# Performance work log

Measured on AMD Instinct MI355X. Metric: run time of the kernel, lower is better.

The kernel has to match this reference:

```python
import jax, jax.numpy as jnp
import numpy as np

NUM_GRAPHS = 512  # number of segments (graphs) in the batch
N_NODES = 200000
HIDDEN = 256


def setup_inputs() -> dict:
    key = jax.random.key(0)
    ks = jax.random.split(key, 8)
    x = jax.random.normal(ks[0], (N_NODES, HIDDEN), dtype=jnp.float32)
    batch = jnp.sort(jax.random.randint(ks[1], (N_NODES,), 0, NUM_GRAPHS, dtype=jnp.int32))
    h4 = HIDDEN // 4
    w1 = jax.random.normal(ks[2], (HIDDEN, h4), dtype=jnp.float32) * (1.0 / np.sqrt(HIDDEN))
    b1 = jnp.zeros((h4,), dtype=jnp.float32)
    w2 = jax.random.normal(ks[3], (h4, 1), dtype=jnp.float32) * (1.0 / np.sqrt(h4))
    b2 = jnp.zeros((1,), dtype=jnp.float32)
    wp = jax.random.normal(ks[4], (3 * HIDDEN, HIDDEN), dtype=jnp.float32) * (1.0 / np.sqrt(3 * HIDDEN))
    bp = jnp.zeros((HIDDEN,), dtype=jnp.float32)
    gamma = jnp.ones((HIDDEN,), dtype=jnp.float32)
    beta = jnp.zeros((HIDDEN,), dtype=jnp.float32)
    return {"x": x, "batch": batch, "w1": w1, "b1": b1, "w2": w2, "b2": b2,
            "wp": wp, "bp": bp, "gamma": gamma, "beta": beta}


def reference(x, batch, w1, b1, w2, b2, wp, bp, gamma, beta):
    G = NUM_GRAPHS
    # --- global mean pool ---
    seg_sum = jax.ops.segment_sum(x, batch, num_segments=G)  # [G, H]
    counts = jax.ops.segment_sum(jnp.ones((x.shape[0],), x.dtype), batch, num_segments=G)
    z_mean = seg_sum / jnp.maximum(counts, 1.0)[:, None]
    # --- global max pool ---
    z_max = jax.ops.segment_max(x, batch, num_segments=G)
    z_max = jnp.where(jnp.isfinite(z_max), z_max, 0.0)  # guard empty segments
    # --- global attention pool (PyG GlobalAttention) ---
    gate = jnp.maximum(x @ w1 + b1, 0.0) @ w2 + b2  # [N, 1]
    g = gate[:, 0]
    g_max = jax.ops.segment_max(g, batch, num_segments=G)
    g_max = jnp.where(jnp.isfinite(g_max), g_max, 0.0)
    e = jnp.exp(g - g_max[batch])
    denom = jax.ops.segment_sum(e, batch, num_segments=G)
    w = e / jnp.maximum(denom, 1e-16)[batch]  # scatter-softmax weights [N]
    z_attn = jax.ops.segment_sum(w[:, None] * x, batch, num_segments=G)
    # --- concat + proj + layernorm ---
    z = jnp.concatenate([z_mean, z_max, z_attn], axis=-1)  # [G, 3H]
    y = z @ wp + bp  # [G, H]
    mu = jnp.mean(y, axis=-1, keepdims=True)
    var = jnp.mean(jnp.square(y - mu), axis=-1, keepdims=True)
    yhat = (y - mu) * jax.lax.rsqrt(var + 1e-5)
    return yhat * gamma + beta
```

## Files before the change

### kernel.cpp

```cpp
#include <hip/hip_runtime.h>
#include <math.h>

#define N_NODES 200000
#define NGRAPH  512
#define HID     256

typedef __attribute__((ext_vector_type(8))) short s16x8;
typedef __attribute__((ext_vector_type(4))) float f32x4;

__device__ __forceinline__ unsigned short f2bf_rne(float f) {
  unsigned int u = __float_as_uint(f);
  return (unsigned short)((u + 0x7fffu + ((u >> 16) & 1u)) >> 16);
}

__global__ __launch_bounds__(256, 2) void fused_gate_pool(
    const float* __restrict__ x,
    const int* __restrict__ batch,
    const float* __restrict__ w1,
    const float* __restrict__ b1,
    const float* __restrict__ w2,
    const float* __restrict__ b2,
    float* __restrict__ zbuf)
{
  __shared__ __align__(16) float chunk_f[64 * 256];
  __shared__ int sbounds[2];
  __shared__ float sm[4], sd[4];

  const int tid = threadIdx.x;
  const int w = tid >> 6;
  const int lane = tid & 63;
  const int q = lane >> 4;
  const int c = lane & 15;

  if (tid < 2) {
    int target = blockIdx.x + tid;
    int lo = 0, hi = N_NODES;
    while (lo < hi) { int mid = (lo + hi) >> 1; if (batch[mid] < target) lo = mid + 1; else hi = mid; }
    sbounds[tid] = lo;
  }

  {
    const float4* src = (const float4*)w1;
    float4* dst = (float4*)chunk_f;
    for (int i = tid; i < 4096; i += 256) dst[i] = src[i];
  }
  __syncthreads();
  s16x8 bh[8][4];
#pragma unroll
  for (int kt = 0; kt < 8; ++kt)
#pragma unroll
    for (int nt = 0; nt < 4; ++nt) {
      s16x8 v;
#pragma unroll
      for (int j = 0; j < 8; ++j)
        v[j] = (short)f2bf_rne(chunk_f[(kt * 32 + q * 8 + j) * 64 + nt * 16 + c]);
      bh[kt][nt] = v;
    }
  float b1v[4], w2v[4];
#pragma unroll
  for (int nt = 0; nt < 4; ++nt) { b1v[nt] = b1[nt * 16 + c]; w2v[nt] = w2[nt * 16 + c]; }
  const float b2v = b2[0];
  const int s = sbounds[0], e = sbounds[1];
  const int cnt = e - s;
  __syncthreads();

  f32x4 sum = (f32x4){0.f, 0.f, 0.f, 0.f};
  f32x4 mx  = (f32x4){-INFINITY, -INFINITY, -INFINITY, -INFINITY};
  f32x4 at  = (f32x4){0.f, 0.f, 0.f, 0.f};
  float den = 0.f, m = -INFINITY;

  const int nchunks = (cnt + 63) >> 6;
  for (int ch = 0; ch < nchunks; ++ch) {
    const int base = s + (ch << 6);
    const int nvalid = min(64, e - base);

#pragma unroll
    for (int it = 0; it < 16; ++it) {
      int row = it * 4 + w;
      if (row < nvalid) {
        const float* gsrc = x + (size_t)(base + row) * HID + lane * 4;
        float* ldst = &chunk_f[row * 256 + lane * 4];
        __builtin_amdgcn_global_load_lds(
            (const __attribute__((address_space(1))) unsigned int*)gsrc,
            (__attribute__((address_space(3))) unsigned int*)ldst, 16, 0, 0);
      }
    }
    __syncthreads();

    const int lim = min(16, nvalid - w * 16);
    if (lim > 0) {
      f32x4 acc[4];
#pragma unroll
      for (int nt = 0; nt < 4; ++nt) acc[nt] = (f32x4){0.f, 0.f, 0.f, 0.f};
#pragma unroll
      for (int kt = 0; kt < 8; ++kt) {
        const float* ar = &chunk_f[(w * 16 + c) * 256 + kt * 32 + q * 8];
        float4 f0 = *(const float4*)ar;
        float4 f1 = *(const float4*)(ar + 4);
        s16x8 ah;
        ah[0] = (short)f2bf_rne(f0.x); ah[1] = (short)f2bf_rne(f0.y);
        ah[2] = (short)f2bf_rne(f0.z); ah[3] = (short)f2bf_rne(f0.w);
        ah[4] = (short)f2bf_rne(f1.x); ah[5] = (short)f2bf_rne(f1.y);
        ah[6] = (short)f2bf_rne(f1.z); ah[7] = (short)f2bf_rne(f1.w);
#pragma unroll
        for (int nt = 0; nt < 4; ++nt)
          acc[nt] = __builtin_amdgcn_mfma_f32_16x16x32_bf16(ah, bh[kt][nt], acc[nt], 0, 0, 0);
      }

      float gr[4];
#pragma unroll
      for (int r = 0; r < 4; ++r) {
        float sv = 0.f;
#pragma unroll
        for (int nt = 0; nt < 4; ++nt) {
          float h = acc[nt][r] + b1v[nt];
          h = h > 0.f ? h : 0.f;
          sv += h * w2v[nt];
        }
        sv += __shfl_xor(sv, 1, 64);
        sv += __shfl_xor(sv, 2, 64);
        sv += __shfl_xor(sv, 4, 64);
        sv += __shfl_xor(sv, 8, 64);
        gr[r] = sv + b2v;
      }

      float gm = -INFINITY;
#pragma unroll
      for (int i = 0; i < 16; ++i) {
        float gv = __shfl(gr[i & 3], (i >> 2) << 4, 64);
        if (i < lim) gm = fmaxf(gm, gv);
      }
      float m_new = fmaxf(m, gm);
      float alpha = (m == -INFINITY) ? 0.f : __expf(m - m_new);
      at = at * alpha;
      den *= alpha;
      m = m_new;

      for (int i = 0; i < lim; ++i) {
        float gv = __shfl(gr[i & 3], (i >> 2) << 4, 64);
        float ei = __expf(gv - m_new);
        den += ei;
        float4 v = *(const float4*)&chunk_f[(w * 16 + i) * 256 + lane * 4];
        f32x4 f = (f32x4){v.x, v.y, v.z, v.w};
        sum = sum + f;
        mx[0] = fmaxf(mx[0], f[0]); mx[1] = fmaxf(mx[1], f[1]);
        mx[2] = fmaxf(mx[2], f[2]); mx[3] = fmaxf(mx[3], f[3]);
        at[0] = fmaf(ei, f[0], at[0]); at[1] = fmaf(ei, f[1], at[1]);
        at[2] = fmaf(ei, f[2], at[2]); at[3] = fmaf(ei, f[3], at[3]);
      }
    }
    __syncthreads();
  }

  {
    float* p0 = &chunk_f[(w * 3 + 0) * 256];
    float* p1 = &chunk_f[(w * 3 + 1) * 256];
    float* p2 = &chunk_f[(w * 3 + 2) * 256];
    int f = lane * 4;
#pragma unroll
    for (int j = 0; j < 4; ++j) { p0[f + j] = sum[j]; p1[f + j] = mx[j]; p2[f + j] = at[j]; }
    if (lane == 0) { sm[w] = m; sd[w] = den; }
  }
  __syncthreads();
  {
    int f = tid;
    float M = fmaxf(fmaxf(sm[0], sm[1]), fmaxf(sm[2], sm[3]));
    float S = 0.f, MX = -INFINITY, A = 0.f, D = 0.f;
#pragma unroll
    for (int ww = 0; ww < 4; ++ww) {
      float sc = (sm[ww] == -INFINITY) ? 0.f : __expf(sm[ww] - M);
      S += chunk_f[(ww * 3 + 0) * 256 + f];
      MX = fmaxf(MX, chunk_f[(ww * 3 + 1) * 256 + f]);
      A = fmaf(sc, chunk_f[(ww * 3 + 2) * 256 + f], A);
      D = fmaf(sc, sd[ww], D);
    }
    float* zr = zbuf + (size_t)blockIdx.x * 768;
    zr[f]       = (cnt > 0) ? S / (float)cnt : 0.f;
    zr[256 + f] = (cnt > 0) ? MX : 0.f;
    zr[512 + f] = (cnt > 0) ? A / fmaxf(D, 1e-16f) : 0.f;
  }
}

__global__ __launch_bounds__(256) void head_ln(
    const float* __restrict__ zbuf,
    const float* __restrict__ wp,
    const float* __restrict__ bp,
    const float* __restrict__ gam,
    const float* __restrict__ bet,
    float* __restrict__ out)
{
  const int g0 = blockIdx.x * 2;
  const int t = threadIdx.x;
  __shared__ float z0[768], z1[768];
  __shared__ f32x4 red[256];
  for (int i = t; i < 768; i += 256) {
    z0[i] = zbuf[(size_t)g0 * 768 + i];
    z1[i] = zbuf[(size_t)(g0 + 1) * 768 + i];
  }
  __syncthreads();

  float a0 = bp[t];
  float a1 = a0;
#pragma unroll 8
  for (int k = 0; k < 768; ++k) {
    float wv = wp[k * 256 + t];
    a0 = fmaf(z0[k], wv, a0);
    a1 = fmaf(z1[k], wv, a1);
  }

  red[t] = (f32x4){a0, a1, 0.f, 0.f};
  __syncthreads();
  for (int wd = 128; wd > 0; wd >>= 1) {
    if (t < wd) red[t] = red[t] + red[t + wd];
    __syncthreads();
  }
  const float inv = 1.f / 256.f;
  float mu0 = red[0].x * inv, mu1 = red[0].y * inv;
  __syncthreads();
  float d0 = a0 - mu0, d1 = a1 - mu1;
  red[t] = (f32x4){d0 * d0, d1 * d1, 0.f, 0.f};
  __syncthreads();
  for (int wd = 128; wd > 0; wd >>= 1) {
    if (t < wd) red[t] = red[t] + red[t + wd];
    __syncthreads();
  }
  float v0 = red[0].x * inv, v1 = red[0].y * inv;
  float is0 = rsqrtf(v0 + 1e-5f);
  float is1 = rsqrtf(v1 + 1e-5f);
  float gv = gam[t], bv = bet[t];
  out[(size_t)g0 * 256 + t]       = fmaf(d0 * is0, gv, bv);
  out[(size_t)(g0 + 1) * 256 + t] = fmaf(d1 * is1, gv, bv);
}

extern "C" void kernel_launch(void* const* d_in, const int* in_sizes, int n_in,
                              void* d_out, int out_size, void* d_ws, size_t ws_size,
                              hipStream_t stream) {
  const float* x   = (const float*)d_in[0];
  const int*   bat = (const int*)d_in[1];
  const float* w1  = (const float*)d_in[2];
  const float* b1  = (const float*)d_in[3];
  const float* w2  = (const float*)d_in[4];
  const float* b2  = (const float*)d_in[5];
  const float* wp  = (const float*)d_in[6];
  const float* bp  = (const float*)d_in[7];
  const float* gam = (const float*)d_in[8];
  const float* bet = (const float*)d_in[9];
  float* out = (float*)d_out;

  float* zbuf = (float*)d_ws;

  hipLaunchKernelGGL(fused_gate_pool, dim3(NGRAPH), dim3(256), 0, stream,
                     x, bat, w1, b1, w2, b2, zbuf);
  hipLaunchKernelGGL(head_ln, dim3(NGRAPH / 2), dim3(256), 0, stream,
                     zbuf, wp, bp, gam, bet, out);
}
```

Before: 390.3 us.

## Split each segment across two blocks, load x directly to registers, add merge kernel

The pooling kernel now launches two blocks per graph, each handling half the segment's rows and writing partial sum/max/attention state plus a softmax max and denominator. A new merge kernel combines the two halves with online-softmax rescaling. Inside the pooling kernel, rows are read straight from global memory into registers and converted to bf16 for MFMA, with no per-chunk LDS staging or barriers. w1 is kept transposed as bf16 in LDS rather than in registers, and occupancy is raised to three blocks per CU. The head kernel now processes one graph per block, splitting K across waves with float4 weight loads. The cost is an extra launch and a partial-state buffer round trip, and each row of x is read twice from global memory.

```diff
diff --git a/kernel.cpp b/kernel.cpp
--- a/kernel.cpp
+++ b/kernel.cpp
@@ -12,136 +12,132 @@
   unsigned int u = __float_as_uint(f);
   return (unsigned short)((u + 0x7fffu + ((u >> 16) & 1u)) >> 16);
 }
-
-__global__ __launch_bounds__(256, 2) void fused_gate_pool(
-    const float* __restrict__ x,
-    const int* __restrict__ batch,
-    const float* __restrict__ w1,
-    const float* __restrict__ b1,
-    const float* __restrict__ w2,
-    const float* __restrict__ b2,
-    float* __restrict__ zbuf)
+__device__ __forceinline__ unsigned int pack2_bf16_rne(float a, float b) {
+  unsigned int ua = __float_as_uint(a), ub = __float_as_uint(b);
+  unsigned int ra = (ua + 0x7fffu + ((ua >> 16) & 1u)) >> 16;
+  unsigned int rb = (ub + 0x7fffu + ((ub >> 16) & 1u)) & 0xffff0000u;
+  return ra | rb;
+}
+
+__global__ __launch_bounds__(256, 3) void pool_partial(
+    const float* __restrict__ x, const int* __restrict__ batch,
+    const float* __restrict__ w1, const float* __restrict__ b1,
+    const float* __restrict__ w2, const float* __restrict__ b2,
+    float* __restrict__ pbuf)
 {
-  __shared__ __align__(16) float chunk_f[64 * 256];
-  __shared__ int sbounds[2];
+  __shared__ __align__(16) short w1T[64 * 264];
+  __shared__ int sb[2];
   __shared__ float sm[4], sd[4];
 
   const int tid = threadIdx.x;
-  const int w = tid >> 6;
-  const int lane = tid & 63;
-  const int q = lane >> 4;
-  const int c = lane & 15;
+  const int w = tid >> 6, lane = tid & 63, q = lane >> 4, c = lane & 15;
+  const int seg = blockIdx.x >> 1, p = blockIdx.x & 1;
 
   if (tid < 2) {
-    int target = blockIdx.x + tid;
+    int target = seg + tid;
     int lo = 0, hi = N_NODES;
     while (lo < hi) { int mid = (lo + hi) >> 1; if (batch[mid] < target) lo = mid + 1; else hi = mid; }
-    sbounds[tid] = lo;
-  }
-
-  {
-    const float4* src = (const float4*)w1;
-    float4* dst = (float4*)chunk_f;
-    for (int i = tid; i < 4096; i += 256) dst[i] = src[i];
-  }
-  __syncthreads();
-  s16x8 bh[8][4];
-#pragma unroll
-  for (int kt = 0; kt < 8; ++kt)
-#pragma unroll
-    for (int nt = 0; nt < 4; ++nt) {
-      s16x8 v;
-#pragma unroll
-      for (int j = 0; j < 8; ++j)
-        v[j] = (short)f2bf_rne(chunk_f[(kt * 32 + q * 8 + j) * 64 + nt * 16 + c]);
-      bh[kt][nt] = v;
-    }
+    sb[tid] = lo;
+  }
+  for (int i = tid; i < 256 * 64; i += 256) {
+    int k = i >> 6, n = i & 63;
+    w1T[n * 264 + k] = (short)f2bf_rne(w1[i]);
+  }
+  __syncthreads();
+
+  const int s0 = sb[0], e0 = sb[1];
+  const int len = e0 - s0;
+  const int ps = s0 + ((len * p) >> 1);
+  const int pe = s0 + ((len * (p + 1)) >> 1);
+  const int plen = pe - ps;
+
   float b1v[4], w2v[4];
 #pragma unroll
   for (int nt = 0; nt < 4; ++nt) { b1v[nt] = b1[nt * 16 + c]; w2v[nt] = w2[nt * 16 + c]; }
   const float b2v = b2[0];
-  const int s = sbounds[0], e = sbounds[1];
-  const int cnt = e - s;
-  __syncthreads();
 
   f32x4 sum = (f32x4){0.f, 0.f, 0.f, 0.f};
   f32x4 mx  = (f32x4){-INFINITY, -INFINITY, -INFINITY, -INFINITY};
   f32x4 at  = (f32x4){0.f, 0.f, 0.f, 0.f};
   float den = 0.f, m = -INFINITY;
 
-  const int nchunks = (cnt + 63) >> 6;
-  for (int ch = 0; ch < nchunks; ++ch) {
-    const int base = s + (ch << 6);
-    const int nvalid = min(64, e - base);
-
-#pragma unroll
-    for (int it = 0; it < 16; ++it) {
-      int row = it * 4 + w;
-      if (row < nvalid) {
-        const float* gsrc = x + (size_t)(base + row) * HID + lane * 4;
-        float* ldst = &chunk_f[row * 256 + lane * 4];
-        __builtin_amdgcn_global_load_lds(
-            (const __attribute__((address_space(1))) unsigned int*)gsrc,
-            (__attribute__((address_space(3))) unsigned int*)ldst, 16, 0, 0);
+  const int ntiles = (plen + 15) >> 4;
+  for (int t = w; t < ntiles; t += 4) {
+    const int r0 = ps + (t << 4);
+    const int lim = min(16, pe - r0);
+
+    const int rowA = r0 + (c < lim ? c : 0);
+    const float* ap = x + (size_t)rowA * HID + q * 8;
+    float4 fa0[8], fa1[8];
+#pragma unroll
+    for (int kt = 0; kt < 8; ++kt) {
+      fa0[kt] = *(const float4*)(ap + kt * 32);
+      fa1[kt] = *(const float4*)(ap + kt * 32 + 4);
+    }
+    union { s16x8 v; unsigned int u[4]; } ah[8];
+#pragma unroll
+    for (int kt = 0; kt < 8; ++kt) {
+      ah[kt].u[0] = pack2_bf16_rne(fa0[kt].x, fa0[kt].y);
+      ah[kt].u[1] = pack2_bf16_rne(fa0[kt].z, fa0[kt].w);
+      ah[kt].u[2] = pack2_bf16_rne(fa1[kt].x, fa1[kt].y);
+      ah[kt].u[3] = pack2_bf16_rne(fa1[kt].z, fa1[kt].w);
+    }
+
+    float4 pv[16];
+#pragma unroll
+    for (int i = 0; i < 16; ++i) {
+      int rr = r0 + (i < lim ? i : 0);
+      pv[i] = *(const float4*)(x + (size_t)rr * HID + lane * 4);
+    }
+
+    f32x4 acc[4];
+#pragma unroll
+    for (int nt = 0; nt < 4; ++nt) acc[nt] = (f32x4){0.f, 0.f, 0.f, 0.f};
+#pragma unroll
+    for (int kt = 0; kt < 8; ++kt) {
+#pragma unroll
+      for (int nt = 0; nt < 4; ++nt) {
+        s16x8 bh = *(const s16x8*)&w1T[(nt * 16 + c) * 264 + kt * 32 + q * 8];
+        acc[nt] = __builtin_amdgcn_mfma_f32_16x16x32_bf16(ah[kt].v, bh, acc[nt], 0, 0, 0);
       }
     }
-    __syncthreads();
-
-    const int lim = min(16, nvalid - w * 16);
-    if (lim > 0) {
-      f32x4 acc[4];
-#pragma unroll
-      for (int nt = 0; nt < 4; ++nt) acc[nt] = (f32x4){0.f, 0.f, 0.f, 0.f};
-#pragma unroll
-      for (int kt = 0; kt < 8; ++kt) {
-        const float* ar = &chunk_f[(w * 16 + c) * 256 + kt * 32 + q * 8];
-        float4 f0 = *(const float4*)ar;
-        float4 f1 = *(const float4*)(ar + 4);
-        s16x8 ah;
-        ah[0] = (short)f2bf_rne(f0.x); ah[1] = (short)f2bf_rne(f0.y);
-        ah[2] = (short)f2bf_rne(f0.z); ah[3] = (short)f2bf_rne(f0.w);
-        ah[4] = (short)f2bf_rne(f1.x); ah[5] = (short)f2bf_rne(f1.y);
-        ah[6] = (short)f2bf_rne(f1.z); ah[7] = (short)f2bf_rne(f1.w);
-#pragma unroll
-        for (int nt = 0; nt < 4; ++nt)
-          acc[nt] = __builtin_amdgcn_mfma_f32_16x16x32_bf16(ah, bh[kt][nt], acc[nt], 0, 0, 0);
+
+    float gr[4];
+#pragma unroll
+    for (int r = 0; r < 4; ++r) {
+      float sv = 0.f;
+#pragma unroll
+      for (int nt = 0; nt < 4; ++nt) {
+        float h = acc[nt][r] + b1v[nt];
+        h = h > 0.f ? h : 0.f;
+        sv += h * w2v[nt];
       }
-
-      float gr[4];
-#pragma unroll
-      for (int r = 0; r < 4; ++r) {
-        float sv = 0.f;
-#pragma unroll
-        for (int nt = 0; nt < 4; ++nt) {
-          float h = acc[nt][r] + b1v[nt];
-          h = h > 0.f ? h : 0.f;
-          sv += h * w2v[nt];
-        }
-        sv += __shfl_xor(sv, 1, 64);
-        sv += __shfl_xor(sv, 2, 64);
-        sv += __shfl_xor(sv, 4, 64);
-        sv += __shfl_xor(sv, 8, 64);
-        gr[r] = sv + b2v;
-      }
-
-      float gm = -INFINITY;
-#pragma unroll
-      for (int i = 0; i < 16; ++i) {
-        float gv = __shfl(gr[i & 3], (i >> 2) << 4, 64);
-        if (i < lim) gm = fmaxf(gm, gv);
-      }
-      float m_new = fmaxf(m, gm);
-      float alpha = (m == -INFINITY) ? 0.f : __expf(m - m_new);
-      at = at * alpha;
-      den *= alpha;
-      m = m_new;
-
-      for (int i = 0; i < lim; ++i) {
-        float gv = __shfl(gr[i & 3], (i >> 2) << 4, 64);
-        float ei = __expf(gv - m_new);
+      sv += __shfl_xor(sv, 1, 64);
+      sv += __shfl_xor(sv, 2, 64);
+      sv += __shfl_xor(sv, 4, 64);
+      sv += __shfl_xor(sv, 8, 64);
+      gr[r] = sv + b2v;
+    }
+
+    float gv16[16];
+    float gm = -INFINITY;
+#pragma unroll
+    for (int i = 0; i < 16; ++i) {
+      gv16[i] = __shfl(gr[i & 3], (i >> 2) << 4, 64);
+      if (i < lim) gm = fmaxf(gm, gv16[i]);
+    }
+    float m_new = fmaxf(m, gm);
+    float alpha = (m == -INFINITY) ? 0.f : __expf(m - m_new);
+    at = at * alpha;
+    den *= alpha;
+    m = m_new;
+
+#pragma unroll
+    for (int i = 0; i < 16; ++i) {
+      if (i < lim) {
+        float ei = __expf(gv16[i] - m_new);
         den += ei;
-        float4 v = *(const float4*)&chunk_f[(w * 16 + i) * 256 + lane * 4];
-        f32x4 f = (f32x4){v.x, v.y, v.z, v.w};
+        f32x4 f = (f32x4){pv[i].x, pv[i].y, pv[i].z, pv[i].w};
         sum = sum + f;
         mx[0] = fmaxf(mx[0], f[0]); mx[1] = fmaxf(mx[1], f[1]);
         mx[2] = fmaxf(mx[2], f[2]); mx[3] = fmaxf(mx[3], f[3]);
@@ -149,13 +145,14 @@
         at[2] = fmaf(ei, f[2], at[2]); at[3] = fmaf(ei, f[3], at[3]);
       }
     }
-    __syncthreads();
-  }
-
+  }
+
+  __syncthreads();
+  float* scr = (float*)w1T;
   {
-    float* p0 = &chunk_f[(w * 3 + 0) * 256];
-    float* p1 = &chunk_f[(w * 3 + 1) * 256];
-    float* p2 = &chunk_f[(w * 3 + 2) * 256];
+    float* p0 = scr + (w * 3 + 0) * 256;
+    float* p1 = scr + (w * 3 + 1) * 256;
+    float* p2 = scr + (w * 3 + 2) * 256;
     int f = lane * 4;
 #pragma unroll
     for (int j = 0; j < 4; ++j) { p0[f + j] = sum[j]; p1[f + j] = mx[j]; p2[f + j] = at[j]; }
@@ -169,67 +166,91 @@
 #pragma unroll
     for (int ww = 0; ww < 4; ++ww) {
       float sc = (sm[ww] == -INFINITY) ? 0.f : __expf(sm[ww] - M);
-      S += chunk_f[(ww * 3 + 0) * 256 + f];
-      MX = fmaxf(MX, chunk_f[(ww * 3 + 1) * 256 + f]);
-      A = fmaf(sc, chunk_f[(ww * 3 + 2) * 256 + f], A);
+      S += scr[(ww * 3 + 0) * 256 + f];
+      MX = fmaxf(MX, scr[(ww * 3 + 1) * 256 + f]);
+      A = fmaf(sc, scr[(ww * 3 + 2) * 256 + f], A);
       D = fmaf(sc, sd[ww], D);
     }
-    float* zr = zbuf + (size_t)blockIdx.x * 768;
-    zr[f]       = (cnt > 0) ? S / (float)cnt : 0.f;
-    zr[256 + f] = (cnt > 0) ? MX : 0.f;
-    zr[512 + f] = (cnt > 0) ? A / fmaxf(D, 1e-16f) : 0.f;
-  }
+    float* pr = pbuf + (size_t)blockIdx.x * 772;
+    pr[f] = S; pr[256 + f] = MX; pr[512 + f] = A;
+    if (tid == 0) { pr[768] = M; pr[769] = D; pr[770] = (float)plen; }
+  }
+}
+
+__global__ __launch_bounds__(256) void pool_merge(
+    const float* __restrict__ pbuf, float* __restrict__ zbuf)
+{
+  const int seg = blockIdx.x;
+  const int f = threadIdx.x;
+  const float* pa = pbuf + (size_t)(seg * 2) * 772;
+  const float* pb = pa + 772;
+  float m0 = pa[768], d0 = pa[769], c0 = pa[770];
+  float m1 = pb[768], d1 = pb[769], c1 = pb[770];
+  float M = fmaxf(m0, m1);
+  float sc0 = (m0 == -INFINITY) ? 0.f : __expf(m0 - M);
+  float sc1 = (m1 == -INFINITY) ? 0.f : __expf(m1 - M);
+  float D = sc0 * d0 + sc1 * d1;
+  float cnt = c0 + c1;
+  float S  = pa[f] + pb[f];
+  float MX = fmaxf(pa[256 + f], pb[256 + f]);
+  float A  = sc0 * pa[512 + f] + sc1 * pb[512 + f];
+  float* zr = zbuf + (size_t)seg * 768;
+  zr[f]       = (cnt > 0.f) ? S / cnt : 0.f;
+  zr[256 + f] = (cnt > 0.f) ? MX : 0.f;
+  zr[512 + f] = (cnt > 0.f) ? A / fmaxf(D, 1e-16f) : 0.f;
 }
 
 __global__ __launch_bounds__(256) void head_ln(
-    const float* __restrict__ zbuf,
-    const float* __restrict__ wp,
-    const float* __restrict__ bp,
-    const float* __restrict__ gam,
-    const float* __restrict__ bet,
-    float* __restrict__ out)
+    const float* __restrict__ zbuf, const float* __restrict__ wp,
+    const float* __restrict__ bp, const float* __restrict__ gam,
+    const float* __restrict__ bet, float* __restrict__ out)
 {
-  const int g0 = blockIdx.x * 2;
-  const int t = threadIdx.x;
-  __shared__ float z0[768], z1[768];
-  __shared__ f32x4 red[256];
-  for (int i = t; i < 768; i += 256) {
-    z0[i] = zbuf[(size_t)g0 * 768 + i];
-    z1[i] = zbuf[(size_t)(g0 + 1) * 768 + i];
-  }
-  __syncthreads();
-
-  float a0 = bp[t];
-  float a1 = a0;
+  const int g = blockIdx.x;
+  const int tid = threadIdx.x;
+  const int w = tid >> 6, lane = tid & 63;
+  __shared__ float z[768];
+  __shared__ __align__(16) float part[4][256];
+  __shared__ float red[256];
+
+  for (int i = tid; i < 768; i += 256) z[i] = zbuf[(size_t)g * 768 + i];
+  __syncthreads();
+
+  f32x4 acc = (f32x4){0.f, 0.f, 0.f, 0.f};
+  const float4* wp4 = (const float4*)wp;
+  const int k0 = w * 192;
 #pragma unroll 8
-  for (int k = 0; k < 768; ++k) {
-    float wv = wp[k * 256 + t];
-    a0 = fmaf(z0[k], wv, a0);
-    a1 = fmaf(z1[k], wv, a1);
-  }
-
-  red[t] = (f32x4){a0, a1, 0.f, 0.f};
+  for (int k = k0; k < k0 + 192; ++k) {
+    float4 wv = wp4[(size_t)k * 64 + lane];
+    float zk = z[k];
+    acc[0] = fmaf(zk, wv.x, acc[0]);
+    acc[1] = fmaf(zk, wv.y, acc[1]);
+    acc[2] = fmaf(zk, wv.z, acc[2]);
+    acc[3] = fmaf(zk, wv.w, acc[3]);
+  }
+  *(f32x4*)&part[w][lane * 4] = acc;
+  __syncthreads();
+
+  const int t = tid;
+  float y = bp[t] + part[0][t] + part[1][t] + part[2][t] + part[3][t];
+
+  red[t] = y;
   __syncthreads();
   for (int wd = 128; wd > 0; wd >>= 1) {
-    if (t < wd) red[t] = red[t] + red[t + wd];
+    if (t < wd) red[t] += red[t + wd];
     __syncthreads();
   }
-  const float inv = 1.f / 256.f;
-  float mu0 = red[0].x * inv, mu1 = red[0].y * inv;
-  __syncthreads();
-  float d0 = a0 - mu0, d1 = a1 - mu1;
-  red[t] = (f32x4){d0 * d0, d1 * d1, 0.f, 0.f};
+  const float mu = red[0] * (1.f / 256.f);
+  __syncthreads();
+  float d = y - mu;
+  red[t] = d * d;
   __syncthreads();
   for (int wd = 128; wd > 0; wd >>= 1) {
-    if (t < wd) red[t] = red[t] + red[t + wd];
+    if (t < wd) red[t] += red[t + wd];
     __syncthreads();
   }
-  float v0 = red[0].x * inv, v1 = red[0].y * inv;
-  float is0 = rsqrtf(v0 + 1e-5f);
-  float is1 = rsqrtf(v1 + 1e-5f);
-  float gv = gam[t], bv = bet[t];
-  out[(size_t)g0 * 256 + t]       = fmaf(d0 * is0, gv, bv);
-  out[(size_t)(g0 + 1) * 256 + t] = fmaf(d1 * is1, gv, bv);
+  const float var = red[0] * (1.f / 256.f);
+  const float is = rsqrtf(var + 1e-5f);
+  out[(size_t)g * 256 + t] = fmaf(d * is, gam[t], bet[t]);
 }
 
 extern "C" void kernel_launch(void* const* d_in, const int* in_sizes, int n_in,
@@ -247,10 +268,12 @@
   const float* bet = (const float*)d_in[9];
   float* out = (float*)d_out;
 
-  float* zbuf = (float*)d_ws;
-
-  hipLaunchKernelGGL(fused_gate_pool, dim3(NGRAPH), dim3(256), 0, stream,
-                     x, bat, w1, b1, w2, b2, zbuf);
-  hipLaunchKernelGGL(head_ln, dim3(NGRAPH / 2), dim3(256), 0, stream,
+  float* pbuf = (float*)d_ws;
+  float* zbuf = (float*)((char*)d_ws + (size_t)1024 * 772 * 4);
+
+  hipLaunchKernelGGL(pool_partial, dim3(NGRAPH * 2), dim3(256), 0, stream,
+                     x, bat, w1, b1, w2, b2, pbuf);
+  hipLaunchKernelGGL(pool_merge, dim3(NGRAPH), dim3(256), 0, stream, pbuf, zbuf);
+  hipLaunchKernelGGL(head_ln, dim3(NGRAPH), dim3(256), 0, stream,
                      zbuf, wp, bp, gam, bet, out);
 }
```

Measured after the change: 437.1 us. 12.0% more time.
